# Kernel optimization log

Hardware: AMD Instinct MI355X
Metric: run time of the kernel (lower is better)

The kernel has to match this reference:

```python
import jax, jax.numpy as jnp
import numpy as np
from jax import lax

RADIUS = 5


def setup_inputs() -> dict:
    key = jax.random.key(0)
    k1, k2 = jax.random.split(key)
    B, K, H, W = 4, 6, 128, 128
    win = 2 * RADIUS + 1
    labels = jax.random.uniform(k1, (B, K, H, W), dtype=jnp.float32)
    weights = jax.random.uniform(k2, (B, H * W, win, win), dtype=jnp.float32)
    return {"labels": labels, "weights": weights}


def reference(labels, weights):
    # labels:  [B, K, H, W]  class probabilities
    B, K, H, W = labels.shape
    win = 2 * RADIUS + 1
    N = H * W

    # Extract 11x11 patches around every pixel for all classes at once.
    patches = lax.conv_general_dilated_patches(
        labels, (win, win), (1, 1), padding=[(RADIUS, RADIUS), (RADIUS, RADIUS)]
    )
    patches = patches.reshape(B, K, win * win, N)

    w = weights.reshape(B, N, win * win)

    # sum over window of weights * P, per class: wp[b,k,n] = sum_o w[b,n,o] * patches[b,k,o,n]
    wp = jnp.einsum('bkon,bno->bkn', patches, w)

    p = labels.reshape(B, K, N)
    num = jnp.einsum('bkn,bkn->bk', p, wp)          # association
    den = jnp.einsum('bkn,bn->bk', p, w.sum(-1))    # degree
    L = num / den                                    # [B, K]

    # nn.L1Loss()(L, zeros) per class = mean_b |L[b,k]|
    losses = jnp.mean(jnp.abs(L), axis=0)            # [K]
    return K - jnp.sum(losses)
```

## Files before the change

### kernel.cpp

```cpp
#include <hip/hip_runtime.h>

#define RADIUS 5
#define WIN    11
#define WIN2   121
#define KCLS   6
#define HH     128
#define WW     128
#define BB     4
#define NPIX   (HH*WW)
#define TPB    256
#define NBLK   (BB*HH*2)
#define PXB    64
#define LABW   (PXB + 2*RADIUS)
#define NSITE  (WIN*LABW)
#define PLSTR  (NSITE*2)

__global__ __launch_bounds__(TPB, 4) void ncut_main(
    const float* __restrict__ labels,
    const float* __restrict__ weights,
    float* __restrict__ part) {
  __shared__ float shl[3 * PLSTR];
  __shared__ float shred[4 * 12];

  const int tid = threadIdx.x;
  const int blk = blockIdx.x;
  const int b   = blk >> 8;
  const int rem = blk & 255;
  const int y0  = rem >> 1;
  const int x0  = (rem & 1) * PXB;

  const float* labB = labels + (size_t)b * KCLS * NPIX;
  for (int s = tid; s < NSITE; s += TPB) {
    const int tr = s / LABW;
    const int tc = s - tr * LABW;
    const int gy = y0 - RADIUS + tr;
    const int gx = x0 + tc - RADIUS;
    const bool ok = ((unsigned)gy < (unsigned)HH) & ((unsigned)gx < (unsigned)WW);
    const float* lp = labB + (size_t)gy * WW + gx;
#pragma unroll
    for (int p = 0; p < 3; ++p) {
      float2 v = make_float2(0.f, 0.f);
      if (ok) {
        v.x = lp[(size_t)(2 * p) * NPIX];
        v.y = lp[(size_t)(2 * p + 1) * NPIX];
      }
      *reinterpret_cast<float2*>(shl + p * PLSTR + 2 * s) = v;
    }
  }
  __syncthreads();

  const int px = tid >> 2;
  const int q  = tid & 3;
  const size_t pxg = (size_t)b * NPIX + (size_t)y0 * WW + x0 + px;
  const int S  = (int)(pxg & 3);
  const float* wal = weights + pxg * WIN2 - S;
  const int T0 = 4 * q - S;

  float2 a0 = make_float2(0.f, 0.f);
  float2 a1 = make_float2(0.f, 0.f);
  float2 a2 = make_float2(0.f, 0.f);
  float wsum = 0.f;

#pragma unroll
  for (int g = 0; g < 8; ++g) {
    const int kq = (g == 7) ? ((q == 3) ? 30 : 28 + q) : 4 * g + q;
    const float4 wv = *reinterpret_cast<const float4*>(wal + 4 * kq);
#pragma unroll
    for (int m = 0; m < 4; ++m) {
      float w = (m == 0) ? wv.x : (m == 1) ? wv.y : (m == 2) ? wv.z : wv.w;
      int   t = 16 * g + m + T0;
      bool valid = true;
      if (g == 0) valid = (q != 0) | (m >= S);
      if (g == 7) valid = (q < 2) | ((q == 2) & (m <= S));
      if (!valid) { w = 0.0f; t = 0; }
      const int r  = (t * 5958) >> 16;
      const int li = px + t + 63 * r;
      const float2 v0 = *reinterpret_cast<const float2*>(shl + 2 * li);
      const float2 v1 = *reinterpret_cast<const float2*>(shl + PLSTR + 2 * li);
      const float2 v2 = *reinterpret_cast<const float2*>(shl + 2 * PLSTR + 2 * li);
      wsum += w;
      a0.x += w * v0.x; a0.y += w * v0.y;
      a1.x += w * v1.x; a1.y += w * v1.y;
      a2.x += w * v2.x; a2.y += w * v2.y;
    }
  }

#pragma unroll
  for (int off = 1; off <= 2; off <<= 1) {
    wsum += __shfl_xor(wsum, off);
    a0.x += __shfl_xor(a0.x, off); a0.y += __shfl_xor(a0.y, off);
    a1.x += __shfl_xor(a1.x, off); a1.y += __shfl_xor(a1.y, off);
    a2.x += __shfl_xor(a2.x, off); a2.y += __shfl_xor(a2.y, off);
  }

  const int lc = px + 5 * LABW + 5;
  const float2 c0 = *reinterpret_cast<const float2*>(shl + 2 * lc);
  const float2 c1 = *reinterpret_cast<const float2*>(shl + PLSTR + 2 * lc);
  const float2 c2 = *reinterpret_cast<const float2*>(shl + 2 * PLSTR + 2 * lc);
  float nv[KCLS] = {c0.x * a0.x, c0.y * a0.y, c1.x * a1.x,
                    c1.y * a1.y, c2.x * a2.x, c2.y * a2.y};
  float dv[KCLS] = {c0.x * wsum, c0.y * wsum, c1.x * wsum,
                    c1.y * wsum, c2.x * wsum, c2.y * wsum};

#pragma unroll
  for (int off = 4; off <= 32; off <<= 1) {
#pragma unroll
    for (int k = 0; k < KCLS; ++k) {
      nv[k] += __shfl_xor(nv[k], off);
      dv[k] += __shfl_xor(dv[k], off);
    }
  }
  const int wave = tid >> 6;
  if ((tid & 63) == 0) {
#pragma unroll
    for (int k = 0; k < KCLS; ++k) {
      shred[wave * 12 + k]     = nv[k];
      shred[wave * 12 + 6 + k] = dv[k];
    }
  }
  __syncthreads();
  if (tid < 12) {
    float s = 0.f;
#pragma unroll
    for (int w = 0; w < 4; ++w) s += shred[w * 12 + tid];
    part[blk * 12 + tid] = s;
  }
}

__global__ __launch_bounds__(256) void ncut_final(
    const float* __restrict__ part, float* __restrict__ out) {
  __shared__ float shf[8 * 48];
  const int t   = threadIdx.x;
  const int seg = t >> 5;
  const int bk  = t & 31;
  if (bk < 24) {
    const int b = bk / KCLS;
    const int k = bk - b * KCLS;
    const int r0 = b * 256 + seg * 32;
    float num = 0.f, den = 0.f;
#pragma unroll 4
    for (int i = 0; i < 32; ++i) {
      const float* p = part + (size_t)(r0 + i) * 12;
      num += p[k];
      den += p[6 + k];
    }
    shf[seg * 48 + bk * 2]     = num;
    shf[seg * 48 + bk * 2 + 1] = den;
  }
  __syncthreads();
  float val = 0.f;
  if (t < 24) {
    float n = 0.f, d = 0.f;
#pragma unroll
    for (int s = 0; s < 8; ++s) {
      n += shf[s * 48 + t * 2];
      d += shf[s * 48 + t * 2 + 1];
    }
    val = fabsf(n / d) * (1.0f / BB);
  }
  if (t < 64) {
#pragma unroll
    for (int off = 16; off; off >>= 1) val += __shfl_down(val, off);
    if (t == 0) out[0] = (float)KCLS - val;
  }
}

extern "C" void kernel_launch(void* const* d_in, const int* in_sizes, int n_in,
                              void* d_out, int out_size, void* d_ws, size_t ws_size,
                              hipStream_t stream) {
  const float* labels  = (const float*)d_in[0];
  const float* weights = (const float*)d_in[1];
  float* out  = (float*)d_out;
  float* part = (float*)d_ws;

  ncut_main<<<NBLK, TPB, 0, stream>>>(labels, weights, part);
  ncut_final<<<1, 256, 0, stream>>>(part, out);
}
```

Measured before the change: 19.81 us.

## Read label windows directly from global memory instead of staging in LDS

Removes the shared-memory staging of the label halo tile and the block-wide barrier, and gathers each window element's six class values straight from global memory, relying on L1/L2 caching. This drops the LDS fill pass and the sync, and may raise occupancy since shared memory use falls. In exchange each thread issues many scattered global loads with per-element bounds checks and offset arithmetic, so gather latency and cache traffic could dominate.

Measured after the change: 36.25 us. 1.83x slower.

```diff
diff --git a/kernel.cpp b/kernel.cpp
--- a/kernel.cpp
+++ b/kernel.cpp
@@ -11,15 +11,11 @@
 #define TPB    256
 #define NBLK   (BB*HH*2)
 #define PXB    64
-#define LABW   (PXB + 2*RADIUS)
-#define NSITE  (WIN*LABW)
-#define PLSTR  (NSITE*2)
 
 __global__ __launch_bounds__(TPB, 4) void ncut_main(
     const float* __restrict__ labels,
     const float* __restrict__ weights,
     float* __restrict__ part) {
-  __shared__ float shl[3 * PLSTR];
   __shared__ float shred[4 * 12];
 
   const int tid = threadIdx.x;
@@ -29,36 +25,17 @@
   const int y0  = rem >> 1;
   const int x0  = (rem & 1) * PXB;
 
-  const float* labB = labels + (size_t)b * KCLS * NPIX;
-  for (int s = tid; s < NSITE; s += TPB) {
-    const int tr = s / LABW;
-    const int tc = s - tr * LABW;
-    const int gy = y0 - RADIUS + tr;
-    const int gx = x0 + tc - RADIUS;
-    const bool ok = ((unsigned)gy < (unsigned)HH) & ((unsigned)gx < (unsigned)WW);
-    const float* lp = labB + (size_t)gy * WW + gx;
-#pragma unroll
-    for (int p = 0; p < 3; ++p) {
-      float2 v = make_float2(0.f, 0.f);
-      if (ok) {
-        v.x = lp[(size_t)(2 * p) * NPIX];
-        v.y = lp[(size_t)(2 * p + 1) * NPIX];
-      }
-      *reinterpret_cast<float2*>(shl + p * PLSTR + 2 * s) = v;
-    }
-  }
-  __syncthreads();
-
   const int px = tid >> 2;
   const int q  = tid & 3;
   const size_t pxg = (size_t)b * NPIX + (size_t)y0 * WW + x0 + px;
   const int S  = (int)(pxg & 3);
   const float* wal = weights + pxg * WIN2 - S;
-  const int T0 = 4 * q - S;
+  const int d  = 4 * q - S;
 
-  float2 a0 = make_float2(0.f, 0.f);
-  float2 a1 = make_float2(0.f, 0.f);
-  float2 a2 = make_float2(0.f, 0.f);
+  const float* lab0 = labels + (size_t)b * KCLS * NPIX;
+  const int gx0 = x0 + px - RADIUS;
+
+  float a0 = 0.f, a1 = 0.f, a2 = 0.f, a3 = 0.f, a4 = 0.f, a5 = 0.f;
   float wsum = 0.f;
 
 #pragma unroll
@@ -67,40 +44,46 @@
     const float4 wv = *reinterpret_cast<const float4*>(wal + 4 * kq);
 #pragma unroll
     for (int m = 0; m < 4; ++m) {
-      float w = (m == 0) ? wv.x : (m == 1) ? wv.y : (m == 2) ? wv.z : wv.w;
-      int   t = 16 * g + m + T0;
-      bool valid = true;
-      if (g == 0) valid = (q != 0) | (m >= S);
-      if (g == 7) valid = (q < 2) | ((q == 2) & (m <= S));
-      if (!valid) { w = 0.0f; t = 0; }
-      const int r  = (t * 5958) >> 16;
-      const int li = px + t + 63 * r;
-      const float2 v0 = *reinterpret_cast<const float2*>(shl + 2 * li);
-      const float2 v1 = *reinterpret_cast<const float2*>(shl + PLSTR + 2 * li);
-      const float2 v2 = *reinterpret_cast<const float2*>(shl + 2 * PLSTR + 2 * li);
-      wsum += w;
-      a0.x += w * v0.x; a0.y += w * v0.y;
-      a1.x += w * v1.x; a1.y += w * v1.y;
-      a2.x += w * v2.x; a2.y += w * v2.y;
+      const float w = (m == 0) ? wv.x : (m == 1) ? wv.y : (m == 2) ? wv.z : wv.w;
+      const int t  = 16 * g + m + d;
+      bool vwin = true;
+      if (g == 0) vwin = (q != 0) | (m >= S);
+      if (g == 7) vwin = (q < 2) | ((q == 2) & (m <= S));
+      const float w0 = vwin ? w : 0.0f;
+      const int tc  = vwin ? t : 0;
+      const int r   = (tc * 5958) >> 16;
+      const int gy  = y0 - RADIUS + r;
+      const int gx  = gx0 + (tc - 11 * r);
+      const bool vi = ((unsigned)gy < (unsigned)HH) & ((unsigned)gx < (unsigned)WW);
+      const int off = vi ? (gy * WW + gx) : 0;
+      const float ww = vi ? w0 : 0.0f;
+      wsum += w0;
+      a0 += ww * lab0[off];
+      a1 += ww * lab0[1 * NPIX + off];
+      a2 += ww * lab0[2 * NPIX + off];
+      a3 += ww * lab0[3 * NPIX + off];
+      a4 += ww * lab0[4 * NPIX + off];
+      a5 += ww * lab0[5 * NPIX + off];
     }
   }
 
 #pragma unroll
   for (int off = 1; off <= 2; off <<= 1) {
     wsum += __shfl_xor(wsum, off);
-    a0.x += __shfl_xor(a0.x, off); a0.y += __shfl_xor(a0.y, off);
-    a1.x += __shfl_xor(a1.x, off); a1.y += __shfl_xor(a1.y, off);
-    a2.x += __shfl_xor(a2.x, off); a2.y += __shfl_xor(a2.y, off);
+    a0 += __shfl_xor(a0, off); a1 += __shfl_xor(a1, off);
+    a2 += __shfl_xor(a2, off); a3 += __shfl_xor(a3, off);
+    a4 += __shfl_xor(a4, off); a5 += __shfl_xor(a5, off);
   }
 
-  const int lc = px + 5 * LABW + 5;
-  const float2 c0 = *reinterpret_cast<const float2*>(shl + 2 * lc);
-  const float2 c1 = *reinterpret_cast<const float2*>(shl + PLSTR + 2 * lc);
-  const float2 c2 = *reinterpret_cast<const float2*>(shl + 2 * PLSTR + 2 * lc);
-  float nv[KCLS] = {c0.x * a0.x, c0.y * a0.y, c1.x * a1.x,
-                    c1.y * a1.y, c2.x * a2.x, c2.y * a2.y};
-  float dv[KCLS] = {c0.x * wsum, c0.y * wsum, c1.x * wsum,
-                    c1.y * wsum, c2.x * wsum, c2.y * wsum};
+  const int coff = y0 * WW + x0 + px;
+  float nv[KCLS], dv[KCLS];
+  const float wpv[KCLS] = {a0, a1, a2, a3, a4, a5};
+#pragma unroll
+  for (int k = 0; k < KCLS; ++k) {
+    const float p = lab0[k * NPIX + coff];
+    nv[k] = p * wpv[k];
+    dv[k] = p * wsum;
+  }
 
 #pragma unroll
   for (int off = 4; off <= 32; off <<= 1) {
```

## Halve pixel tile per block and transpose partials for vectorized final reduction

Applied to the files above, without the earlier changes.

Each block of the main kernel now covers 32 pixels with 128 threads instead of 64 pixels with 256, which doubles the block count to 2048 and gives more scheduling granularity on the many CUs. Per-block partials are written in slot-major layout, so the final kernel can read contiguous float4 runs with 4 segments per sum. The smaller tile increases halo overhead: label staging per output pixel rises from 74/64 to 42/32 columns, and the final kernel has twice as many partials to reduce.

New measurement: 19.04 us, median of 2. 3.8% less time.

```diff
diff --git a/kernel.cpp b/kernel.cpp
--- a/kernel.cpp
+++ b/kernel.cpp
@@ -8,9 +8,9 @@
 #define WW     128
 #define BB     4
 #define NPIX   (HH*WW)
-#define TPB    256
-#define NBLK   (BB*HH*2)
-#define PXB    64
+#define TPB    128
+#define PXB    32
+#define NBLK   (BB*HH*(WW/PXB))
 #define LABW   (PXB + 2*RADIUS)
 #define NSITE  (WIN*LABW)
 #define PLSTR  (NSITE*2)
@@ -20,14 +20,14 @@
     const float* __restrict__ weights,
     float* __restrict__ part) {
   __shared__ float shl[3 * PLSTR];
-  __shared__ float shred[4 * 12];
+  __shared__ float shred[2 * 12];
 
   const int tid = threadIdx.x;
   const int blk = blockIdx.x;
-  const int b   = blk >> 8;
-  const int rem = blk & 255;
-  const int y0  = rem >> 1;
-  const int x0  = (rem & 1) * PXB;
+  const int b   = blk >> 9;
+  const int rem = blk & 511;
+  const int y0  = rem >> 2;
+  const int x0  = (rem & 3) * PXB;
 
   const float* labB = labels + (size_t)b * KCLS * NPIX;
   for (int s = tid; s < NSITE; s += TPB) {
@@ -74,7 +74,7 @@
       if (g == 7) valid = (q < 2) | ((q == 2) & (m <= S));
       if (!valid) { w = 0.0f; t = 0; }
       const int r  = (t * 5958) >> 16;
-      const int li = px + t + 63 * r;
+      const int li = px + t + (LABW - WIN) * r;
       const float2 v0 = *reinterpret_cast<const float2*>(shl + 2 * li);
       const float2 v1 = *reinterpret_cast<const float2*>(shl + PLSTR + 2 * li);
       const float2 v2 = *reinterpret_cast<const float2*>(shl + 2 * PLSTR + 2 * li);
@@ -120,47 +120,45 @@
   }
   __syncthreads();
   if (tid < 12) {
-    float s = 0.f;
-#pragma unroll
-    for (int w = 0; w < 4; ++w) s += shred[w * 12 + tid];
-    part[blk * 12 + tid] = s;
+    part[tid * NBLK + blk] = shred[tid] + shred[12 + tid];
   }
 }
 
 __global__ __launch_bounds__(256) void ncut_final(
     const float* __restrict__ part, float* __restrict__ out) {
-  __shared__ float shf[8 * 48];
-  const int t   = threadIdx.x;
-  const int seg = t >> 5;
-  const int bk  = t & 31;
-  if (bk < 24) {
-    const int b = bk / KCLS;
-    const int k = bk - b * KCLS;
-    const int r0 = b * 256 + seg * 32;
-    float num = 0.f, den = 0.f;
-#pragma unroll 4
+  __shared__ float shf[4 * 48];
+  const int t     = threadIdx.x;
+  const int sumid = t >> 2;
+  const int seg   = t & 3;
+  if (sumid < 48) {
+    const int isden = sumid / 24;
+    const int bk    = sumid - isden * 24;
+    const int b     = bk / KCLS;
+    const int k     = bk - b * KCLS;
+    const int slot  = isden * KCLS + k;
+    const float* p  = part + (size_t)slot * NBLK + b * (NBLK / BB) + seg * 128;
+    float s = 0.f;
+#pragma unroll 8
     for (int i = 0; i < 32; ++i) {
-      const float* p = part + (size_t)(r0 + i) * 12;
-      num += p[k];
-      den += p[6 + k];
+      const float4 v = *reinterpret_cast<const float4*>(p + 4 * i);
+      s += v.x + v.y + v.z + v.w;
     }
-    shf[seg * 48 + bk * 2]     = num;
-    shf[seg * 48 + bk * 2 + 1] = den;
+    shf[seg * 48 + sumid] = s;
   }
   __syncthreads();
   float val = 0.f;
   if (t < 24) {
-    float n = 0.f, d = 0.f;
+    float num = 0.f, den = 0.f;
 #pragma unroll
-    for (int s = 0; s < 8; ++s) {
-      n += shf[s * 48 + t * 2];
-      d += shf[s * 48 + t * 2 + 1];
+    for (int sg = 0; sg < 4; ++sg) {
+      num += shf[sg * 48 + t];
+      den += shf[sg * 48 + 24 + t];
     }
-    val = fabsf(n / d) * (1.0f / BB);
+    val = fabsf(num / den) * (1.0f / BB);
   }
   if (t < 64) {
 #pragma unroll
-    for (int off = 16; off; off >>= 1) val += __shfl_down(val, off);
+    for (int off = 32; off; off >>= 1) val += __shfl_down(val, off);
     if (t == 0) out[0] = (float)KCLS - val;
   }
 }
```
